# Kernel tuning notes

Hardware: AMD Instinct MI355X
Metric: run time of the kernel (lower is better)

The kernel has to match this reference:

```python
import jax, jax.numpy as jnp
import numpy as np

# TT decomposition config (from Eff_TTEmbedding args in source)
P = (216, 216, 216)      # auto-factorized p_shapes for n=10,000,000 (216^3 >= n)
Q = (2, 4, 2)            # tt_q_shapes, prod = 16 = embedding_dim
R = (128, 128)           # tt_ranks
NUM_TABLES = 2
BATCH = 1024
NUM_EMB = 10_000_000


def setup_inputs() -> dict:
    key = jax.random.key(0)
    k0, k1, k2, k3 = jax.random.split(key, 4)
    # sparse indices per TT table: [n_tables, batch]
    lS_i = jax.random.randint(k3, (NUM_TABLES, BATCH), 0, NUM_EMB, dtype=jnp.int64)
    # TT cores, weight_dist='uniform'
    core0 = jax.random.uniform(k0, (NUM_TABLES, P[0], Q[0] * R[0]), dtype=jnp.float32, minval=-0.01, maxval=0.01)
    core1 = jax.random.uniform(k1, (NUM_TABLES, P[1], R[0] * Q[1] * R[1]), dtype=jnp.float32, minval=-0.01, maxval=0.01)
    core2 = jax.random.uniform(k2, (NUM_TABLES, P[2], R[1] * Q[2]), dtype=jnp.float32, minval=-0.01, maxval=0.01)
    return {"lS_i": lS_i, "core0": core0, "core1": core1, "core2": core2}


def _tt_lookup(idx, c0, c1, c2):
    """TT embedding lookup for one table. idx: [B] int; returns [B, prod(Q)]."""
    B = idx.shape[0]
    # mixed-radix decomposition of flat index into (i0, i1, i2)
    i0 = idx // (P[1] * P[2])
    i1 = (idx // P[2]) % P[1]
    i2 = idx % P[2]
    # gather TT core slices (the memory-bound irregular access)
    A = c0[i0].reshape(B, Q[0], R[0])            # [B, 2, 128]
    Bm = c1[i1].reshape(B, R[0], Q[1] * R[1])    # [B, 128, 512]
    C = c2[i2].reshape(B, R[1], Q[2])            # [B, 128, 2]
    # chained small matmuls along TT ranks
    AB = jnp.einsum('bqr,brs->bqs', A, Bm).reshape(B, Q[0] * Q[1], R[1])  # [B, 8, 128]
    out = jnp.einsum('bqr,brs->bqs', AB, C)      # [B, 8, 2]
    return out.reshape(B, Q[0] * Q[1] * Q[2])    # [B, 16]


def reference(lS_i, core0, core1, core2):
    # per-table dispatch (forward returns one embedding bag per TT table)
    return jax.vmap(_tt_lookup)(lS_i, core0, core1, core2)  # [n_tables, B, 16]
```

## Files before the change

### kernel.cpp

```cpp
#include <hip/hip_runtime.h>


#define CAP 128

__global__ __launch_bounds__(128) void tt_fused(
    const int* __restrict__ idx32,
    const float* __restrict__ c0,
    const float* __restrict__ c1,
    const float* __restrict__ c2,
    float* __restrict__ out)
{
    const int g     = blockIdx.x;
    const int q     = blockIdx.y;
    const int table = g / 216;
    const int i1    = g - table * 216;

    const int tid = threadIdx.x;
    const int rh  = tid >> 6;
    const int tl  = tid & 63;

    __shared__ float lds[4096];
    __shared__ int s_id[CAP];
    __shared__ int s_aux[CAP];
    __shared__ int s_cnt;

    if (tid == 0) s_cnt = 0;
    __syncthreads();

    const bool is64 = (idx32[1] == 0) & (idx32[3] == 0) &
                      (idx32[5] == 0) & (idx32[7] == 0);

    for (int j = tid; j < 1024; j += 128) {
        const int id = (table << 10) + j;
        const unsigned idx = is64 ? (unsigned)((const long long*)idx32)[id]
                                  : (unsigned)idx32[id];
        const unsigned i0  = idx / 46656u;
        const unsigned rem = idx - i0 * 46656u;
        const unsigned bi1 = rem / 216u;
        if ((int)bi1 == i1) {
            const unsigned i2 = rem - bi1 * 216u;
            const int pos = atomicAdd(&s_cnt, 1);
            if (pos < CAP) {
                s_id[pos]  = id;
                s_aux[pos] = (int)((i0 << 16) | i2);
            }
        }
    }
    __syncthreads();
    const int m = min(s_cnt, CAP);
    if (m == 0) return;

    float2*       lds2 = (float2*)lds;
    const float4* lds4 = (const float4*)lds;

    const float2* b2 = (const float2*)(c1 + ((size_t)g << 16))
                       + (size_t)rh * 64 * 256 + (q * 64 + tl);
    const float* c0t = c0 + (size_t)table * 216 * 256;

    for (int base = 0; base < m; base += 8) {
        const int cl = min(8, m - base);
        __syncthreads();

        for (int l = 0; l < cl; ++l) {
            const float* ar = c0t + (size_t)(s_aux[base + l] >> 16) * 256;
#pragma unroll
            for (int k = 0; k < 2; ++k) {
                const int e = tid + 128 * k;
                lds[l * 256 + 2 * (e & 127) + (e >> 7)] = ar[e];
            }
        }
        __syncthreads();

        float2 acc[8][2];
#pragma unroll
        for (int l = 0; l < 8; ++l) {
            acc[l][0] = make_float2(0.f, 0.f);
            acc[l][1] = make_float2(0.f, 0.f);
        }

#pragma unroll 8
        for (int rr2 = 0; rr2 < 32; ++rr2) {
            const float2 bv0 = b2[(size_t)(2 * rr2) * 256];
            const float2 bv1 = b2[(size_t)(2 * rr2 + 1) * 256];
            const int rhalf = rh * 32 + rr2;
#pragma unroll
            for (int l = 0; l < 8; ++l) {
                const float4 av = lds4[l * 64 + rhalf];
                acc[l][0].x += av.x * bv0.x; acc[l][0].y += av.x * bv0.y;
                acc[l][1].x += av.y * bv0.x; acc[l][1].y += av.y * bv0.y;
                acc[l][0].x += av.z * bv1.x; acc[l][0].y += av.z * bv1.y;
                acc[l][1].x += av.w * bv1.x; acc[l][1].y += av.w * bv1.y;
            }
        }

        __syncthreads();
#pragma unroll
        for (int l = 0; l < 8; ++l) {
            lds2[((rh * 8 + l) * 2 + 0) * 64 + tl] = acc[l][0];
            lds2[((rh * 8 + l) * 2 + 1) * 64 + tl] = acc[l][1];
        }
        __syncthreads();

#pragma unroll
        for (int ll = 0; ll < 4; ++ll) {
            const int l = 2 * ll + rh;
            if (l < cl) {
                const float2 u0 = lds2[((0 * 8 + l) * 2 + 0) * 64 + tl];
                const float2 u1 = lds2[((1 * 8 + l) * 2 + 0) * 64 + tl];
                const float2 v0 = lds2[((0 * 8 + l) * 2 + 1) * 64 + tl];
                const float2 v1 = lds2[((1 * 8 + l) * 2 + 1) * 64 + tl];
                const float a0x = u0.x + u1.x, a0y = u0.y + u1.y;
                const float a1x = v0.x + v1.x, a1y = v0.y + v1.y;
                const float* crow = c2 + (size_t)(table * 216 + (s_aux[base + l] & 0xffff)) * 256;
                const float4 cv = *(const float4*)(crow + 4 * tl);
                float p00 = a0x * cv.x + a0y * cv.z;
                float p01 = a0x * cv.y + a0y * cv.w;
                float p10 = a1x * cv.x + a1y * cv.z;
                float p11 = a1x * cv.y + a1y * cv.w;
#pragma unroll
                for (int mm = 32; mm >= 1; mm >>= 1) {
                    p00 += __shfl_xor(p00, mm);
                    p01 += __shfl_xor(p01, mm);
                    p10 += __shfl_xor(p10, mm);
                    p11 += __shfl_xor(p11, mm);
                }
                if (tl == 0) {
                    float* o = out + (size_t)s_id[base + l] * 16;
                    *(float2*)(o + q * 2)     = make_float2(p00, p01);
                    *(float2*)(o + 8 + q * 2) = make_float2(p10, p11);
                }
            }
        }
    }
}

extern "C" void kernel_launch(void* const* d_in, const int* in_sizes, int n_in,
                              void* d_out, int out_size, void* d_ws, size_t ws_size,
                              hipStream_t stream) {
    const int*   idx = (const int*)d_in[0];
    const float* c0  = (const float*)d_in[1];
    const float* c1  = (const float*)d_in[2];
    const float* c2  = (const float*)d_in[3];
    float* out = (float*)d_out;
    (void)d_ws; (void)ws_size; (void)in_sizes; (void)n_in; (void)out_size;

    tt_fused<<<dim3(432, 4), dim3(128), 0, stream>>>(idx, c0, c1, c2, out);
}
```

Measured before the change: 194.0 us.

## Split per-slice rows across two blocks and use ballot-based compaction

Adds a z-dimension of two blocks per (i1, q) group, each handling alternating chunks of eight matching rows, which doubles the number of blocks doing the c1 slice work. Row compaction now uses a single wave with ballot/popcount instead of shared-memory atomics. The cross-half reduction is done by having one half write to LDS and the other add its registers, which halves LDS use. CAP drops to 48, so a slice with more matches than that would silently lose rows, and every extra block re-reads the indices and the c1 slice.

```diff
diff --git a/kernel.cpp b/kernel.cpp
--- a/kernel.cpp
+++ b/kernel.cpp
@@ -1,7 +1,7 @@
 #include <hip/hip_runtime.h>
 
 
-#define CAP 128
+#define CAP 48
 
 __global__ __launch_bounds__(128) void tt_fused(
     const int* __restrict__ idx32,
@@ -12,6 +12,7 @@
 {
     const int g     = blockIdx.x;
     const int q     = blockIdx.y;
+    const int cs    = blockIdx.z;
     const int table = g / 216;
     const int i1    = g - table * 216;
 
@@ -19,36 +20,44 @@
     const int rh  = tid >> 6;
     const int tl  = tid & 63;
 
-    __shared__ float lds[4096];
+    __shared__ float lds[2048];
     __shared__ int s_id[CAP];
     __shared__ int s_aux[CAP];
     __shared__ int s_cnt;
 
-    if (tid == 0) s_cnt = 0;
-    __syncthreads();
+    if (tid < CAP) s_aux[tid] = 0;
 
     const bool is64 = (idx32[1] == 0) & (idx32[3] == 0) &
                       (idx32[5] == 0) & (idx32[7] == 0);
 
-    for (int j = tid; j < 1024; j += 128) {
-        const int id = (table << 10) + j;
-        const unsigned idx = is64 ? (unsigned)((const long long*)idx32)[id]
-                                  : (unsigned)idx32[id];
-        const unsigned i0  = idx / 46656u;
-        const unsigned rem = idx - i0 * 46656u;
-        const unsigned bi1 = rem / 216u;
-        if ((int)bi1 == i1) {
-            const unsigned i2 = rem - bi1 * 216u;
-            const int pos = atomicAdd(&s_cnt, 1);
-            if (pos < CAP) {
-                s_id[pos]  = id;
-                s_aux[pos] = (int)((i0 << 16) | i2);
+    if (rh == 0) {
+        int cnt = 0;
+#pragma unroll 4
+        for (int it = 0; it < 16; ++it) {
+            const int j  = it * 64 + tl;
+            const int id = (table << 10) + j;
+            const unsigned idx = is64 ? (unsigned)((const long long*)idx32)[id]
+                                      : (unsigned)idx32[id];
+            const unsigned i0  = idx / 46656u;
+            const unsigned rem = idx - i0 * 46656u;
+            const unsigned bi1 = rem / 216u;
+            const bool match = ((int)bi1 == i1);
+            const unsigned long long mask = __ballot(match);
+            if (match) {
+                const int pos = cnt + __popcll(mask & ((1ull << tl) - 1ull));
+                if (pos < CAP) {
+                    const unsigned i2 = rem - bi1 * 216u;
+                    s_id[pos]  = id;
+                    s_aux[pos] = (int)((i0 << 16) | i2);
+                }
             }
+            cnt += (int)__popcll(mask);
         }
+        if (tl == 0) s_cnt = cnt;
     }
     __syncthreads();
     const int m = min(s_cnt, CAP);
-    if (m == 0) return;
+    if (m <= cs * 8) return;
 
     float2*       lds2 = (float2*)lds;
     const float4* lds4 = (const float4*)lds;
@@ -57,11 +66,12 @@
                        + (size_t)rh * 64 * 256 + (q * 64 + tl);
     const float* c0t = c0 + (size_t)table * 216 * 256;
 
-    for (int base = 0; base < m; base += 8) {
+    for (int base = cs * 8; base < m; base += 16) {
         const int cl = min(8, m - base);
         __syncthreads();
 
-        for (int l = 0; l < cl; ++l) {
+#pragma unroll
+        for (int l = 0; l < 8; ++l) {
             const float* ar = c0t + (size_t)(s_aux[base + l] >> 16) * 256;
 #pragma unroll
             for (int k = 0; k < 2; ++k) {
@@ -94,40 +104,42 @@
         }
 
         __syncthreads();
+        if (rh == 1) {
 #pragma unroll
-        for (int l = 0; l < 8; ++l) {
-            lds2[((rh * 8 + l) * 2 + 0) * 64 + tl] = acc[l][0];
-            lds2[((rh * 8 + l) * 2 + 1) * 64 + tl] = acc[l][1];
+            for (int l = 0; l < 8; ++l) {
+                lds2[(l * 2 + 0) * 64 + tl] = acc[l][0];
+                lds2[(l * 2 + 1) * 64 + tl] = acc[l][1];
+            }
         }
         __syncthreads();
 
+        if (rh == 0) {
 #pragma unroll
-        for (int ll = 0; ll < 4; ++ll) {
-            const int l = 2 * ll + rh;
-            if (l < cl) {
-                const float2 u0 = lds2[((0 * 8 + l) * 2 + 0) * 64 + tl];
-                const float2 u1 = lds2[((1 * 8 + l) * 2 + 0) * 64 + tl];
-                const float2 v0 = lds2[((0 * 8 + l) * 2 + 1) * 64 + tl];
-                const float2 v1 = lds2[((1 * 8 + l) * 2 + 1) * 64 + tl];
-                const float a0x = u0.x + u1.x, a0y = u0.y + u1.y;
-                const float a1x = v0.x + v1.x, a1y = v0.y + v1.y;
-                const float* crow = c2 + (size_t)(table * 216 + (s_aux[base + l] & 0xffff)) * 256;
-                const float4 cv = *(const float4*)(crow + 4 * tl);
-                float p00 = a0x * cv.x + a0y * cv.z;
-                float p01 = a0x * cv.y + a0y * cv.w;
-                float p10 = a1x * cv.x + a1y * cv.z;
-                float p11 = a1x * cv.y + a1y * cv.w;
+            for (int l = 0; l < 8; ++l) {
+                const float2 t0 = lds2[(l * 2 + 0) * 64 + tl];
+                const float2 t1 = lds2[(l * 2 + 1) * 64 + tl];
+                const float a0x = acc[l][0].x + t0.x, a0y = acc[l][0].y + t0.y;
+                const float a1x = acc[l][1].x + t1.x, a1y = acc[l][1].y + t1.y;
+                if (l < cl) {
+                    const float* crow =
+                        c2 + (size_t)(table * 216 + (s_aux[base + l] & 0xffff)) * 256;
+                    const float4 cv = *(const float4*)(crow + 4 * tl);
+                    float p00 = a0x * cv.x + a0y * cv.z;
+                    float p01 = a0x * cv.y + a0y * cv.w;
+                    float p10 = a1x * cv.x + a1y * cv.z;
+                    float p11 = a1x * cv.y + a1y * cv.w;
 #pragma unroll
-                for (int mm = 32; mm >= 1; mm >>= 1) {
-                    p00 += __shfl_xor(p00, mm);
-                    p01 += __shfl_xor(p01, mm);
-                    p10 += __shfl_xor(p10, mm);
-                    p11 += __shfl_xor(p11, mm);
-                }
-                if (tl == 0) {
-                    float* o = out + (size_t)s_id[base + l] * 16;
-                    *(float2*)(o + q * 2)     = make_float2(p00, p01);
-                    *(float2*)(o + 8 + q * 2) = make_float2(p10, p11);
+                    for (int mm = 32; mm >= 1; mm >>= 1) {
+                        p00 += __shfl_xor(p00, mm);
+                        p01 += __shfl_xor(p01, mm);
+                        p10 += __shfl_xor(p10, mm);
+                        p11 += __shfl_xor(p11, mm);
+                    }
+                    if (tl == 0) {
+                        float* o = out + (size_t)s_id[base + l] * 16;
+                        *(float2*)(o + q * 2)     = make_float2(p00, p01);
+                        *(float2*)(o + 8 + q * 2) = make_float2(p10, p11);
+                    }
                 }
             }
         }
@@ -144,5 +156,5 @@
     float* out = (float*)d_out;
     (void)d_ws; (void)ws_size; (void)in_sizes; (void)n_in; (void)out_size;
 
-    tt_fused<<<dim3(432, 4), dim3(128), 0, stream>>>(idx, c0, c1, c2, out);
+    tt_fused<<<dim3(432, 4, 2), dim3(128), 0, stream>>>(idx, c0, c1, c2, out);
 }
```

Result: no change. 191.3 us (-1.4%).
